# Performance work log

Hardware: AMD Instinct MI355X
Metric: run time of the kernel (lower is better)

Reference implementation:

```python
import jax, jax.numpy as jnp
import numpy as np

NB, NA, NC, NH, NW = 32, 5, 80, 64, 64
MAXT = 50
STRIDE = 32.0
ANCHORS_PX = [42.3, 55.4, 102.2, 128.3, 161.8, 259.2, 303.1, 154.9, 359.6, 320.2]
NOOBJECT_SCALE, OBJECT_SCALE = 1.0, 5.0
COORD_SCALE, CLASS_SCALE = 1.0, 1.0
SIL_THRESH = 0.6


def _iou_center(ax, ay, aw, ah, bx, by, bw, bh):
    # IoU for boxes in (cx, cy, w, h) form; zero when no overlap (matches bbox_ious x1y1x2y2=False)
    iw = jnp.minimum(ax + aw * 0.5, bx + bw * 0.5) - jnp.maximum(ax - aw * 0.5, bx - bw * 0.5)
    ih = jnp.minimum(ay + ah * 0.5, by + bh * 0.5) - jnp.maximum(ay - ah * 0.5, by - bh * 0.5)
    inter = jnp.maximum(iw, 0.0) * jnp.maximum(ih, 0.0)
    union = aw * ah + bw * bh - inter
    return inter / union


def _region_loss(output, target):
    sg = jax.lax.stop_gradient
    anchors = jnp.array(ANCHORS_PX, jnp.float32).reshape(NA, 2) / STRIDE  # anchors scaled by stride
    out = output.reshape(NB, NA, 5 + NC, NH, NW)
    x = jax.nn.sigmoid(out[:, :, 0])
    y = jax.nn.sigmoid(out[:, :, 1])
    w = out[:, :, 2]
    h = out[:, :, 3]
    conf = jax.nn.sigmoid(out[:, :, 4])
    cls_logits = jnp.transpose(out[:, :, 5:], (0, 1, 3, 4, 2))  # [B,A,H,W,C]

    grid_x = jnp.arange(NW, dtype=jnp.float32)[None, None, None, :]
    grid_y = jnp.arange(NH, dtype=jnp.float32)[None, None, :, None]
    aw = anchors[:, 0][None, :, None, None]
    ah = anchors[:, 1][None, :, None, None]
    # decoded pred boxes are detached in the torch code (built from .data)
    px = sg(x) + grid_x
    py = sg(y) + grid_y
    pw = jnp.exp(sg(w)) * aw
    ph = jnp.exp(sg(h)) * ah

    tgt = sg(target).reshape(NB, MAXT, 5)  # [cls, x, y, w, h] per target, normalized
    gcls = tgt[:, :, 0]
    gx = tgt[:, :, 1] * NW
    gy = tgt[:, :, 2] * NH
    gw = tgt[:, :, 3] * NW
    gh = tgt[:, :, 4] * NH
    # loop breaks at first target with x == 0 -> cumulative validity
    valid = jnp.cumprod((tgt[:, :, 1] != 0).astype(jnp.float32), axis=1) > 0  # [B,T]

    # --- conf mask silencing: max IoU of each pred box against all GT boxes ---
    ious = _iou_center(px[..., None], py[..., None], pw[..., None], ph[..., None],
                       gx[:, None, None, None, :], gy[:, None, None, None, :],
                       gw[:, None, None, None, :], gh[:, None, None, None, :])  # [B,A,H,W,T]
    ious = jnp.where(valid[:, None, None, None, :], ious, 0.0)
    cur_ious = jnp.max(ious, axis=-1)
    conf_mask0 = jnp.where(cur_ious > SIL_THRESH, 0.0, NOOBJECT_SCALE)

    # --- best anchor per GT: wh-only IoU at origin (anchor_step == 2) ---
    inter = jnp.minimum(gw[..., None], anchors[None, None, :, 0]) * \
            jnp.minimum(gh[..., None], anchors[None, None, :, 1])  # [B,T,A]
    union = gw[..., None] * gh[..., None] + anchors[None, None, :, 0] * anchors[None, None, :, 1] - inter
    best_n = jnp.argmax(inter / union, axis=-1)

    gi = jnp.clip(gx.astype(jnp.int32), 0, NW - 1)
    gj = jnp.clip(gy.astype(jnp.int32), 0, NH - 1)
    bidx = jnp.arange(NB, dtype=jnp.int32)[:, None]
    aw_b = anchors[best_n, 0]
    ah_b = anchors[best_n, 1]

    pb_x = px[bidx, best_n, gj, gi]
    pb_y = py[bidx, best_n, gj, gi]
    pb_w = pw[bidx, best_n, gj, gi]
    pb_h = ph[bidx, best_n, gj, gi]
    t_iou = _iou_center(gx, gy, gw, gh, pb_x, pb_y, pb_w, pb_h)  # [B,T]

    N = NB * NA * NH * NW
    flat = ((bidx * NA + best_n) * NH + gj) * NW + gi
    flat = jnp.where(valid, flat, N).reshape(-1)  # invalid targets scattered to dummy slot

    def scat(base, vals):
        padded = jnp.concatenate([base.reshape(-1), jnp.zeros((1,), base.dtype)])
        return padded.at[flat].set(vals.reshape(-1))[:N].reshape(NB, NA, NH, NW)

    ones_t = jnp.ones_like(gx)
    # seen=0 < 12800 -> coord_mask = 1 everywhere, tx=ty=0.5, tw=th=0 as base
    coord_mask = scat(jnp.ones((NB, NA, NH, NW), jnp.float32), ones_t)
    cls_mask = scat(jnp.zeros((NB, NA, NH, NW), jnp.float32), ones_t)
    conf_mask = scat(conf_mask0, jnp.full_like(gx, OBJECT_SCALE))
    txg = scat(jnp.full((NB, NA, NH, NW), 0.5, jnp.float32), gx - gi.astype(jnp.float32))
    tyg = scat(jnp.full((NB, NA, NH, NW), 0.5, jnp.float32), gy - gj.astype(jnp.float32))
    twg = scat(jnp.zeros((NB, NA, NH, NW), jnp.float32), jnp.log(gw / aw_b))
    thg = scat(jnp.zeros((NB, NA, NH, NW), jnp.float32), jnp.log(gh / ah_b))
    tconf = scat(jnp.zeros((NB, NA, NH, NW), jnp.float32), t_iou)
    tcls = scat(jnp.zeros((NB, NA, NH, NW), jnp.float32), gcls)

    conf_m = jnp.sqrt(conf_mask)
    loss_x = COORD_SCALE * jnp.sum((x * coord_mask - txg * coord_mask) ** 2) / 2.0
    loss_y = COORD_SCALE * jnp.sum((y * coord_mask - tyg * coord_mask) ** 2) / 2.0
    loss_w = COORD_SCALE * jnp.sum((w * coord_mask - twg * coord_mask) ** 2) / 2.0
    loss_h = COORD_SCALE * jnp.sum((h * coord_mask - thg * coord_mask) ** 2) / 2.0
    loss_conf = jnp.sum((conf * conf_m - tconf * conf_m) ** 2) / 2.0
    # CrossEntropy over cells where cls_mask == 1 (sum reduction)
    logZ = jax.nn.logsumexp(cls_logits, axis=-1)
    picked = jnp.take_along_axis(cls_logits, tcls.astype(jnp.int32)[..., None], axis=-1)[..., 0]
    loss_cls = CLASS_SCALE * jnp.sum((logZ - picked) * cls_mask)
    return loss_x + loss_y + loss_w + loss_h + loss_conf + loss_cls


def setup_inputs() -> dict:
    key = jax.random.key(0)
    k1, k2, k3, k4 = jax.random.split(key, 4)
    output = jax.random.normal(k1, (NB, NA * (5 + NC), NH, NW), jnp.float32) * 0.5
    cls_ids = jax.random.randint(k2, (NB, MAXT), 0, NC).astype(jnp.float32)
    xy = jax.random.uniform(k3, (NB, MAXT, 2), jnp.float32, minval=0.05, maxval=0.95)
    wh = jax.random.uniform(k4, (NB, MAXT, 2), jnp.float32, minval=0.05, maxval=0.4)
    target = jnp.concatenate([cls_ids[..., None], xy, wh], axis=-1).reshape(NB, MAXT * 5)
    return {"output": output, "target": target}


def reference(output, target):
    return _region_loss(output, target)
```

## Files before the change

kernel.cpp:

```cpp
#include <hip/hip_runtime.h>

#define NB 32
#define NA 5
#define NC 80
#define NH 64
#define NW 64
#define MAXT 50
#define CH 85
#define HW (NH*NW)
#define NCELL (NB*NA*HW)

#define TGT_BASE 16
#define TGT_STRIDE 336
#define ENT_BASE (TGT_BASE + NB*TGT_STRIDE)
#define ENT_STRIDE (8 + 8*MAXT)
#define T_XLO 16
#define T_XHI 80
#define T_YLO 144
#define T_YHI 208
#define T_GA  272

__constant__ float c_aw[NA] = {42.3f/32.0f, 102.2f/32.0f, 161.8f/32.0f, 303.1f/32.0f, 359.6f/32.0f};
__constant__ float c_ah[NA] = {55.4f/32.0f, 128.3f/32.0f, 259.2f/32.0f, 154.9f/32.0f, 320.2f/32.0f};

__device__ __forceinline__ float sigm(float x) {
    return __builtin_amdgcn_rcpf(1.0f + __expf(-x));
}

__global__ void prep_kernel(const float* __restrict__ out, const float* __restrict__ tgt,
                            float* __restrict__ W) {
    const int b = blockIdx.x;
    const int t = threadIdx.x;
    if (b == 0 && t == 0) W[0] = 0.0f;

    __shared__ int s_id[MAXT];

    bool iszero = true;
    float gcls = 0.f, gx = 0.f, gy = 0.f, gw = 0.f, gh = 0.f;
    if (t < MAXT) {
        const float* p = tgt + (b*MAXT + t)*5;
        gcls = p[0];
        float rx = p[1];
        iszero = (rx == 0.0f);
        gx = rx * (float)NW;
        gy = p[2] * (float)NH;
        gw = p[3] * (float)NW;
        gh = p[4] * (float)NH;
    }
    unsigned long long mz = __ballot(iszero);
    const int nvalid = __ffsll(mz) - 1;

    float* TB = W + TGT_BASE + (size_t)b*TGT_STRIDE;

    int   myid = -1;
    float tx = 0.f, ty = 0.f, tw = 0.f, th = 0.f, tiou = 0.f;
    int   mycl = 0;

    if (t < MAXT) {
        TB[T_XLO + t] = gx - 0.5f*gw;
        TB[T_XHI + t] = gx + 0.5f*gw;
        TB[T_YLO + t] = gy - 0.5f*gh;
        TB[T_YHI + t] = gy + 0.5f*gh;
        TB[T_GA  + t] = 0.375f * gw * gh;

        float garea = gw * gh;
        float best = -1.0f; int bn = 0;
        #pragma unroll
        for (int n = 0; n < NA; n++) {
            float inter = fminf(gw, c_aw[n]) * fminf(gh, c_ah[n]);
            float uni = garea + c_aw[n]*c_ah[n] - inter;
            float r = inter / uni;
            if (r > best) { best = r; bn = n; }
        }
        int gi = (int)gx; gi = gi < 0 ? 0 : (gi > NW-1 ? NW-1 : gi);
        int gj = (int)gy; gj = gj < 0 ? 0 : (gj > NH-1 ? NH-1 : gj);
        float awb = c_aw[bn], ahb = c_ah[bn];

        int base = ((b*NA + bn)*CH)*HW + gj*NW + gi;
        float ox = out[base];
        float oy = out[base + HW];
        float ow = out[base + 2*HW];
        float oh = out[base + 3*HW];
        float px = sigm(ox) + (float)gi;
        float py = sigm(oy) + (float)gj;
        float pw = __expf(ow) * awb;
        float ph = __expf(oh) * ahb;
        float iw = fminf(gx + 0.5f*gw, px + 0.5f*pw) - fmaxf(gx - 0.5f*gw, px - 0.5f*pw);
        float ih = fminf(gy + 0.5f*gh, py + 0.5f*ph) - fmaxf(gy - 0.5f*gh, py - 0.5f*ph);
        float inter = fmaxf(iw, 0.f) * fmaxf(ih, 0.f);
        tiou = inter / (garea + pw*ph - inter);

        myid = (bn*NH + gj)*NW + gi;
        tx = gx - (float)gi;
        ty = gy - (float)gj;
        tw = __logf(gw / awb);
        th = __logf(gh / ahb);
        mycl = (int)gcls;
        s_id[t] = myid;
    }
    __syncthreads();

    bool keepf = (t < nvalid);
    if (keepf) {
        for (int u = t + 1; u < nvalid; u++) {
            if (s_id[u] == myid) { keepf = false; break; }
        }
    }

    float* EB = W + ENT_BASE + (size_t)b*ENT_STRIDE;
    if (t == 0) {
        ((int*)TB)[0] = nvalid;
        ((int*)EB)[0] = nvalid;
    }
    if (t < nvalid) {
        float* e = EB + 8 + t*8;
        ((int*)e)[0] = keepf ? myid : -1;
        e[1] = tx; e[2] = ty; e[3] = tw; e[4] = th; e[5] = tiou;
        ((int*)e)[6] = mycl;
    }
}

__global__ __launch_bounds__(256) void main_kernel(const float* __restrict__ out,
                                                   float* __restrict__ W) {
    const int cell = blockIdx.x * 256 + threadIdx.x;
    const int b = cell / (NA*HW);
    const int rem = cell - b*(NA*HW);
    const int a = rem / HW;
    const int ji = rem & (HW-1);
    const int i = ji & (NW-1);
    const int j = ji >> 6;

    __shared__ float sxl[MAXT], sxh[MAXT], syl[MAXT], syh[MAXT], sga[MAXT];
    __shared__ int s_nv;
    const float* TB = W + TGT_BASE + (size_t)b*TGT_STRIDE;
    if (threadIdx.x == 0) s_nv = ((const int*)TB)[0];
    if (threadIdx.x < MAXT) {
        int t = threadIdx.x;
        sxl[t] = TB[T_XLO+t]; sxh[t] = TB[T_XHI+t];
        syl[t] = TB[T_YLO+t]; syh[t] = TB[T_YHI+t];
        sga[t] = TB[T_GA+t];
    }
    __syncthreads();

    const size_t base = (size_t)((b*NA + a)*CH)*HW + ji;
    const float ox = out[base];
    const float oy = out[base + HW];
    const float ow = out[base + 2*HW];
    const float oh = out[base + 3*HW];
    const float oc = out[base + 4*HW];

    const float sx = sigm(ox);
    const float sy = sigm(oy);
    const float sc = sigm(oc);
    const float pw = __expf(ow) * c_aw[a];
    const float ph = __expf(oh) * c_ah[a];
    const float px = sx + (float)i;
    const float py = sy + (float)j;
    const float pxl = px - 0.5f*pw, pxh = px + 0.5f*pw;
    const float pyl = py - 0.5f*ph, pyh = py + 0.5f*ph;
    const float pa375 = 0.375f * pw * ph;

    const int nv = s_nv;
    float m = -1.0f;
    for (int tt = 0; tt < nv; tt++) {
        float iw = fminf(pxh, sxh[tt]) - fmaxf(pxl, sxl[tt]);
        float ih = fminf(pyh, syh[tt]) - fmaxf(pyl, syl[tt]);
        float inter = fmaxf(iw, 0.f) * fmaxf(ih, 0.f);
        m = fmaxf(m, inter - sga[tt]);
    }
    const bool over = m > pa375;

    const float dx = sx - 0.5f, dy = sy - 0.5f;
    float v = dx*dx + dy*dy + ow*ow + oh*oh;
    if (!over) v += sc*sc;
    v *= 0.5f;

    for (int off = 32; off > 0; off >>= 1) v += __shfl_down(v, off);
    __shared__ float red[4];
    if ((threadIdx.x & 63) == 0) red[threadIdx.x >> 6] = v;
    __syncthreads();
    if (threadIdx.x == 0) atomicAdd(W, red[0]+red[1]+red[2]+red[3]);
}

__global__ void corr_kernel(const float* __restrict__ out, float* __restrict__ W) {
    const int b = blockIdx.x;
    const int t = threadIdx.x;
    __shared__ float sxl[MAXT], sxh[MAXT], syl[MAXT], syh[MAXT], sga[MAXT];
    const float* TB = W + TGT_BASE + (size_t)b*TGT_STRIDE;
    const int nv = ((const int*)TB)[0];
    if (t < MAXT) {
        sxl[t] = TB[T_XLO+t]; sxh[t] = TB[T_XHI+t];
        syl[t] = TB[T_YLO+t]; syh[t] = TB[T_YHI+t];
        sga[t] = TB[T_GA+t];
    }
    __syncthreads();
    const float* EB = W + ENT_BASE + (size_t)b*ENT_STRIDE;
    const int cnt = ((const int*)EB)[0];
    float acc = 0.f;
    for (int e = t; e < cnt; e += 64) {
        const float* en = EB + 8 + e*8;
        const int id = ((const int*)en)[0];
        if (id < 0) continue;
        const float tx = en[1], ty = en[2], tw = en[3], th = en[4], ti = en[5];
        const int cls = ((const int*)en)[6];
        const int a = id >> 12;
        const int ji = id & (HW-1);
        const int i = ji & (NW-1);
        const int j = ji >> 6;
        const size_t base = (size_t)((b*NA + a)*CH)*HW + ji;
        const float ox = out[base];
        const float oy = out[base + HW];
        const float ow = out[base + 2*HW];
        const float oh = out[base + 3*HW];
        const float oc = out[base + 4*HW];
        const float sx = sigm(ox), sy = sigm(oy), sc = sigm(oc);

        const float dxn = sx - tx, dxo = sx - 0.5f;
        const float dyn = sy - ty, dyo = sy - 0.5f;
        const float dwn = ow - tw, dhn = oh - th;
        float d = dxn*dxn - dxo*dxo + dyn*dyn - dyo*dyo + dwn*dwn - ow*ow + dhn*dhn - oh*oh;

        const float pw = __expf(ow) * c_aw[a];
        const float ph = __expf(oh) * c_ah[a];
        const float px = sx + (float)i, py = sy + (float)j;
        const float pxl = px - 0.5f*pw, pxh = px + 0.5f*pw;
        const float pyl = py - 0.5f*ph, pyh = py + 0.5f*ph;
        const float pa375 = 0.375f * pw * ph;
        float mm = -1.0f;
        for (int u = 0; u < nv; u++) {
            float iw = fminf(pxh, sxh[u]) - fmaxf(pxl, sxl[u]);
            float ih = fminf(pyh, syh[u]) - fmaxf(pyl, syl[u]);
            float inter = fmaxf(iw, 0.f) * fmaxf(ih, 0.f);
            mm = fmaxf(mm, inter - sga[u]);
        }
        float dc = 5.f*(sc - ti)*(sc - ti);
        if (!(mm > pa375)) dc -= sc*sc;
        d += dc;
        acc += 0.5f * d;

        const float* lg = out + base + 5*HW;
        float mx = lg[0];
        for (int c = 1; c < NC; c++) mx = fmaxf(mx, lg[(size_t)c*HW]);
        float s = 0.f;
        for (int c = 0; c < NC; c++) s += __expf(lg[(size_t)c*HW] - mx);
        acc += mx + __logf(s) - lg[(size_t)cls*HW];
    }
    for (int off = 32; off > 0; off >>= 1) acc += __shfl_down(acc, off);
    if (t == 0) atomicAdd(W, acc);
}

__global__ void fin_kernel(const float* __restrict__ W, float* __restrict__ res) {
    res[0] = W[0];
}

extern "C" void kernel_launch(void* const* d_in, const int* in_sizes, int n_in,
                              void* d_out, int out_size, void* d_ws, size_t ws_size,
                              hipStream_t stream) {
    const float* out = (const float*)d_in[0];
    const float* tgt = (const float*)d_in[1];
    float* W = (float*)d_ws;
    float* res = (float*)d_out;
    hipLaunchKernelGGL(prep_kernel, dim3(NB), dim3(64), 0, stream, out, tgt, W);
    hipLaunchKernelGGL(main_kernel, dim3(NCELL/256), dim3(256), 0, stream, out, W);
    hipLaunchKernelGGL(corr_kernel, dim3(NB), dim3(64), 0, stream, out, W);
    hipLaunchKernelGGL(fin_kernel, dim3(1), dim3(1), 0, stream, W, res);
}
```

Baseline: 331.7 us.

## Fuse prep, main and correction kernels into one pass with per-block partials

Merges the target-prep, per-cell conf loss, and per-target correction kernels into a single kernel. Each block recomputes target boxes in shared memory, and the first block of each image also does the correction work, splitting the class logsumexp across 4 lanes per target. The global atomic is replaced by per-block partial sums that a final kernel reduces. This removes two launches and the serial correction kernel, but every block now redundantly reads the targets and the r==0 blocks carry extra work.

```diff
diff --git a/kernel.cpp b/kernel.cpp
--- a/kernel.cpp
+++ b/kernel.cpp
@@ -8,17 +8,8 @@
 #define MAXT 50
 #define CH 85
 #define HW (NH*NW)
-#define NCELL (NB*NA*HW)
-
-#define TGT_BASE 16
-#define TGT_STRIDE 336
-#define ENT_BASE (TGT_BASE + NB*TGT_STRIDE)
-#define ENT_STRIDE (8 + 8*MAXT)
-#define T_XLO 16
-#define T_XHI 80
-#define T_YLO 144
-#define T_YHI 208
-#define T_GA  272
+#define NBLK (NB*NA*HW/256)
+#define BPB (NA*HW/256)
 
 __constant__ float c_aw[NA] = {42.3f/32.0f, 102.2f/32.0f, 161.8f/32.0f, 303.1f/32.0f, 359.6f/32.0f};
 __constant__ float c_ah[NA] = {55.4f/32.0f, 128.3f/32.0f, 259.2f/32.0f, 154.9f/32.0f, 320.2f/32.0f};
@@ -27,120 +18,48 @@
     return __builtin_amdgcn_rcpf(1.0f + __expf(-x));
 }
 
-__global__ void prep_kernel(const float* __restrict__ out, const float* __restrict__ tgt,
-                            float* __restrict__ W) {
-    const int b = blockIdx.x;
-    const int t = threadIdx.x;
-    if (b == 0 && t == 0) W[0] = 0.0f;
-
-    __shared__ int s_id[MAXT];
-
-    bool iszero = true;
-    float gcls = 0.f, gx = 0.f, gy = 0.f, gw = 0.f, gh = 0.f;
-    if (t < MAXT) {
-        const float* p = tgt + (b*MAXT + t)*5;
-        gcls = p[0];
-        float rx = p[1];
-        iszero = (rx == 0.0f);
-        gx = rx * (float)NW;
-        gy = p[2] * (float)NH;
-        gw = p[3] * (float)NW;
-        gh = p[4] * (float)NH;
-    }
-    unsigned long long mz = __ballot(iszero);
-    const int nvalid = __ffsll(mz) - 1;
-
-    float* TB = W + TGT_BASE + (size_t)b*TGT_STRIDE;
-
-    int   myid = -1;
-    float tx = 0.f, ty = 0.f, tw = 0.f, th = 0.f, tiou = 0.f;
-    int   mycl = 0;
-
-    if (t < MAXT) {
-        TB[T_XLO + t] = gx - 0.5f*gw;
-        TB[T_XHI + t] = gx + 0.5f*gw;
-        TB[T_YLO + t] = gy - 0.5f*gh;
-        TB[T_YHI + t] = gy + 0.5f*gh;
-        TB[T_GA  + t] = 0.375f * gw * gh;
-
-        float garea = gw * gh;
-        float best = -1.0f; int bn = 0;
-        #pragma unroll
-        for (int n = 0; n < NA; n++) {
-            float inter = fminf(gw, c_aw[n]) * fminf(gh, c_ah[n]);
-            float uni = garea + c_aw[n]*c_ah[n] - inter;
-            float r = inter / uni;
-            if (r > best) { best = r; bn = n; }
-        }
-        int gi = (int)gx; gi = gi < 0 ? 0 : (gi > NW-1 ? NW-1 : gi);
-        int gj = (int)gy; gj = gj < 0 ? 0 : (gj > NH-1 ? NH-1 : gj);
-        float awb = c_aw[bn], ahb = c_ah[bn];
-
-        int base = ((b*NA + bn)*CH)*HW + gj*NW + gi;
-        float ox = out[base];
-        float oy = out[base + HW];
-        float ow = out[base + 2*HW];
-        float oh = out[base + 3*HW];
-        float px = sigm(ox) + (float)gi;
-        float py = sigm(oy) + (float)gj;
-        float pw = __expf(ow) * awb;
-        float ph = __expf(oh) * ahb;
-        float iw = fminf(gx + 0.5f*gw, px + 0.5f*pw) - fmaxf(gx - 0.5f*gw, px - 0.5f*pw);
-        float ih = fminf(gy + 0.5f*gh, py + 0.5f*ph) - fmaxf(gy - 0.5f*gh, py - 0.5f*ph);
-        float inter = fmaxf(iw, 0.f) * fmaxf(ih, 0.f);
-        tiou = inter / (garea + pw*ph - inter);
-
-        myid = (bn*NH + gj)*NW + gi;
-        tx = gx - (float)gi;
-        ty = gy - (float)gj;
-        tw = __logf(gw / awb);
-        th = __logf(gh / ahb);
-        mycl = (int)gcls;
-        s_id[t] = myid;
+__global__ __launch_bounds__(256) void fused_kernel(const float* __restrict__ out,
+                                                    const float* __restrict__ tgt,
+                                                    float* __restrict__ W) {
+    const int blk = blockIdx.x;
+    const int tid = threadIdx.x;
+    const int b   = blk / BPB;
+    const int r   = blk - b*BPB;
+    const int a   = r >> 4;
+    const int ji  = ((r & 15) << 8) + tid;
+    const int i   = ji & (NW-1);
+    const int j   = ji >> 6;
+
+    __shared__ float sxl[MAXT], sxh[MAXT], syl[MAXT], syh[MAXT], sga[MAXT];
+    __shared__ float sgx[MAXT], sgy[MAXT], sgw[MAXT], sgh[MAXT], sgc[MAXT];
+    __shared__ int   s_id[MAXT];
+    __shared__ int   s_eid[MAXT];
+    __shared__ float s_tx[MAXT], s_ty[MAXT], s_tw[MAXT], s_th[MAXT], s_ti[MAXT];
+    __shared__ int   s_ec[MAXT];
+    __shared__ int   s_nv;
+    __shared__ float red[4];
+
+    if (tid < 64) {
+        bool iszero = true;
+        if (tid < MAXT) {
+            const float* p = tgt + (b*MAXT + tid)*5;
+            const float gcls = p[0];
+            const float rx = p[1];
+            iszero = (rx == 0.0f);
+            const float gx = rx   * (float)NW;
+            const float gy = p[2] * (float)NH;
+            const float gw = p[3] * (float)NW;
+            const float gh = p[4] * (float)NH;
+            sxl[tid] = gx - 0.5f*gw; sxh[tid] = gx + 0.5f*gw;
+            syl[tid] = gy - 0.5f*gh; syh[tid] = gy + 0.5f*gh;
+            sga[tid] = 0.375f*gw*gh;
+            sgx[tid] = gx; sgy[tid] = gy; sgw[tid] = gw; sgh[tid] = gh; sgc[tid] = gcls;
+        }
+        unsigned long long mz = __ballot(iszero);
+        if (tid == 0) s_nv = __ffsll(mz) - 1;
     }
     __syncthreads();
-
-    bool keepf = (t < nvalid);
-    if (keepf) {
-        for (int u = t + 1; u < nvalid; u++) {
-            if (s_id[u] == myid) { keepf = false; break; }
-        }
-    }
-
-    float* EB = W + ENT_BASE + (size_t)b*ENT_STRIDE;
-    if (t == 0) {
-        ((int*)TB)[0] = nvalid;
-        ((int*)EB)[0] = nvalid;
-    }
-    if (t < nvalid) {
-        float* e = EB + 8 + t*8;
-        ((int*)e)[0] = keepf ? myid : -1;
-        e[1] = tx; e[2] = ty; e[3] = tw; e[4] = th; e[5] = tiou;
-        ((int*)e)[6] = mycl;
-    }
-}
-
-__global__ __launch_bounds__(256) void main_kernel(const float* __restrict__ out,
-                                                   float* __restrict__ W) {
-    const int cell = blockIdx.x * 256 + threadIdx.x;
-    const int b = cell / (NA*HW);
-    const int rem = cell - b*(NA*HW);
-    const int a = rem / HW;
-    const int ji = rem & (HW-1);
-    const int i = ji & (NW-1);
-    const int j = ji >> 6;
-
-    __shared__ float sxl[MAXT], sxh[MAXT], syl[MAXT], syh[MAXT], sga[MAXT];
-    __shared__ int s_nv;
-    const float* TB = W + TGT_BASE + (size_t)b*TGT_STRIDE;
-    if (threadIdx.x == 0) s_nv = ((const int*)TB)[0];
-    if (threadIdx.x < MAXT) {
-        int t = threadIdx.x;
-        sxl[t] = TB[T_XLO+t]; sxh[t] = TB[T_XHI+t];
-        syl[t] = TB[T_YLO+t]; syh[t] = TB[T_YHI+t];
-        sga[t] = TB[T_GA+t];
-    }
-    __syncthreads();
+    const int nv = s_nv;
 
     const size_t base = (size_t)((b*NA + a)*CH)*HW + ji;
     const float ox = out[base];
@@ -160,7 +79,6 @@
     const float pyl = py - 0.5f*ph, pyh = py + 0.5f*ph;
     const float pa375 = 0.375f * pw * ph;
 
-    const int nv = s_nv;
     float m = -1.0f;
     for (int tt = 0; tt < nv; tt++) {
         float iw = fminf(pxh, sxh[tt]) - fmaxf(pxl, sxl[tt]);
@@ -176,81 +94,141 @@
     v *= 0.5f;
 
     for (int off = 32; off > 0; off >>= 1) v += __shfl_down(v, off);
+    if ((tid & 63) == 0) red[tid >> 6] = v;
+    __syncthreads();
+    float bsum = (tid == 0) ? (red[0] + red[1] + red[2] + red[3]) : 0.0f;
+
+    if (r == 0) {
+        if (tid < 64 && tid < nv) {
+            const float gx = sgx[tid], gy = sgy[tid], gw = sgw[tid], gh = sgh[tid];
+            const float garea = gw * gh;
+            float best = -1.0f; int bn = 0;
+            #pragma unroll
+            for (int n = 0; n < NA; n++) {
+                float inter = fminf(gw, c_aw[n]) * fminf(gh, c_ah[n]);
+                float uni = garea + c_aw[n]*c_ah[n] - inter;
+                float rr = inter / uni;
+                if (rr > best) { best = rr; bn = n; }
+            }
+            int gi = (int)gx; gi = gi < 0 ? 0 : (gi > NW-1 ? NW-1 : gi);
+            int gj = (int)gy; gj = gj < 0 ? 0 : (gj > NH-1 ? NH-1 : gj);
+            const float awb = c_aw[bn], ahb = c_ah[bn];
+
+            const size_t gbase = (size_t)((b*NA + bn)*CH)*HW + gj*NW + gi;
+            const float o0 = out[gbase];
+            const float o1 = out[gbase + HW];
+            const float o2 = out[gbase + 2*HW];
+            const float o3 = out[gbase + 3*HW];
+            const float ppx = sigm(o0) + (float)gi;
+            const float ppy = sigm(o1) + (float)gj;
+            const float ppw = __expf(o2) * awb;
+            const float pph = __expf(o3) * ahb;
+            const float iw = fminf(gx + 0.5f*gw, ppx + 0.5f*ppw) - fmaxf(gx - 0.5f*gw, ppx - 0.5f*ppw);
+            const float ih = fminf(gy + 0.5f*gh, ppy + 0.5f*pph) - fmaxf(gy - 0.5f*gh, ppy - 0.5f*pph);
+            const float inter = fmaxf(iw, 0.f) * fmaxf(ih, 0.f);
+            const float tiou = inter / (garea + ppw*pph - inter);
+
+            s_id[tid] = (bn*NH + gj)*NW + gi;
+            s_tx[tid] = gx - (float)gi;
+            s_ty[tid] = gy - (float)gj;
+            s_tw[tid] = __logf(gw / awb);
+            s_th[tid] = __logf(gh / ahb);
+            s_ti[tid] = tiou;
+            s_ec[tid] = (int)sgc[tid];
+        }
+        __syncthreads();
+        if (tid < nv) {
+            const int myid = s_id[tid];
+            bool keep = true;
+            for (int u = tid + 1; u < nv; u++)
+                if (s_id[u] == myid) { keep = false; break; }
+            s_eid[tid] = keep ? myid : -1;
+        }
+        __syncthreads();
+
+        float acc = 0.0f;
+        const int e = tid >> 2;
+        const int q = tid & 3;
+        if (e < nv) {
+            const int id = s_eid[e];
+            if (id >= 0) {
+                const int ea  = id >> 12;
+                const int eji = id & (HW-1);
+                const int eii = eji & (NW-1);
+                const int ejj = eji >> 6;
+                const size_t eb = (size_t)((b*NA + ea)*CH)*HW + eji;
+                const float cox = out[eb];
+                const float coy = out[eb + HW];
+                const float cow = out[eb + 2*HW];
+                const float coh = out[eb + 3*HW];
+                const float coc = out[eb + 4*HW];
+                const float csx = sigm(cox), csy = sigm(coy), csc = sigm(coc);
+                const float cpw = __expf(cow) * c_aw[ea];
+                const float cph = __expf(coh) * c_ah[ea];
+                const float cpx = csx + (float)eii, cpy = csy + (float)ejj;
+                const float cxl = cpx - 0.5f*cpw, cxh = cpx + 0.5f*cpw;
+                const float cyl = cpy - 0.5f*cph, cyh = cpy + 0.5f*cph;
+                const float cpa = 0.375f * cpw * cph;
+
+                float mm = -1.0f;
+                for (int u = q; u < nv; u += 4) {
+                    float iw = fminf(cxh, sxh[u]) - fmaxf(cxl, sxl[u]);
+                    float ih = fminf(cyh, syh[u]) - fmaxf(cyl, syl[u]);
+                    float inter = fmaxf(iw, 0.f) * fmaxf(ih, 0.f);
+                    mm = fmaxf(mm, inter - sga[u]);
+                }
+                mm = fmaxf(mm, __shfl_xor(mm, 1));
+                mm = fmaxf(mm, __shfl_xor(mm, 2));
+
+                const float* lg = out + eb + 5*HW;
+                float rch[20];
+                #pragma unroll
+                for (int k = 0; k < 20; k++) rch[k] = lg[(size_t)(q + 4*k)*HW];
+                float mx = rch[0];
+                #pragma unroll
+                for (int k = 1; k < 20; k++) mx = fmaxf(mx, rch[k]);
+                mx = fmaxf(mx, __shfl_xor(mx, 1));
+                mx = fmaxf(mx, __shfl_xor(mx, 2));
+                float s = 0.0f;
+                #pragma unroll
+                for (int k = 0; k < 20; k++) s += __expf(rch[k] - mx);
+                s += __shfl_xor(s, 1);
+                s += __shfl_xor(s, 2);
+
+                if (q == 0) {
+                    const float tx = s_tx[e], ty = s_ty[e], tw = s_tw[e], th = s_th[e], ti = s_ti[e];
+                    const int cls = s_ec[e];
+                    const float dxn = csx - tx, dxo = csx - 0.5f;
+                    const float dyn = csy - ty, dyo = csy - 0.5f;
+                    const float dwn = cow - tw, dhn = coh - th;
+                    float d = dxn*dxn - dxo*dxo + dyn*dyn - dyo*dyo
+                            + dwn*dwn - cow*cow + dhn*dhn - coh*coh;
+                    float dc = 5.f*(csc - ti)*(csc - ti);
+                    if (!(mm > cpa)) dc -= csc*csc;
+                    d += dc;
+                    acc += 0.5f * d;
+                    acc += mx + __logf(s) - lg[(size_t)cls*HW];
+                }
+            }
+        }
+        for (int off = 32; off > 0; off >>= 1) acc += __shfl_down(acc, off);
+        if ((tid & 63) == 0) red[tid >> 6] = acc;
+        __syncthreads();
+        if (tid == 0) bsum += red[0] + red[1] + red[2] + red[3];
+    }
+
+    if (tid == 0) W[blk] = bsum;
+}
+
+__global__ __launch_bounds__(256) void fin_kernel(const float* __restrict__ W,
+                                                  float* __restrict__ res) {
+    float s = 0.0f;
+    for (int k = threadIdx.x; k < NBLK; k += 256) s += W[k];
+    for (int off = 32; off > 0; off >>= 1) s += __shfl_down(s, off);
     __shared__ float red[4];
-    if ((threadIdx.x & 63) == 0) red[threadIdx.x >> 6] = v;
+    if ((threadIdx.x & 63) == 0) red[threadIdx.x >> 6] = s;
     __syncthreads();
-    if (threadIdx.x == 0) atomicAdd(W, red[0]+red[1]+red[2]+red[3]);
-}
-
-__global__ void corr_kernel(const float* __restrict__ out, float* __restrict__ W) {
-    const int b = blockIdx.x;
-    const int t = threadIdx.x;
-    __shared__ float sxl[MAXT], sxh[MAXT], syl[MAXT], syh[MAXT], sga[MAXT];
-    const float* TB = W + TGT_BASE + (size_t)b*TGT_STRIDE;
-    const int nv = ((const int*)TB)[0];
-    if (t < MAXT) {
-        sxl[t] = TB[T_XLO+t]; sxh[t] = TB[T_XHI+t];
-        syl[t] = TB[T_YLO+t]; syh[t] = TB[T_YHI+t];
-        sga[t] = TB[T_GA+t];
-    }
-    __syncthreads();
-    const float* EB = W + ENT_BASE + (size_t)b*ENT_STRIDE;
-    const int cnt = ((const int*)EB)[0];
-    float acc = 0.f;
-    for (int e = t; e < cnt; e += 64) {
-        const float* en = EB + 8 + e*8;
-        const int id = ((const int*)en)[0];
-        if (id < 0) continue;
-        const float tx = en[1], ty = en[2], tw = en[3], th = en[4], ti = en[5];
-        const int cls = ((const int*)en)[6];
-        const int a = id >> 12;
-        const int ji = id & (HW-1);
-        const int i = ji & (NW-1);
-        const int j = ji >> 6;
-        const size_t base = (size_t)((b*NA + a)*CH)*HW + ji;
-        const float ox = out[base];
-        const float oy = out[base + HW];
-        const float ow = out[base + 2*HW];
-        const float oh = out[base + 3*HW];
-        const float oc = out[base + 4*HW];
-        const float sx = sigm(ox), sy = sigm(oy), sc = sigm(oc);
-
-        const float dxn = sx - tx, dxo = sx - 0.5f;
-        const float dyn = sy - ty, dyo = sy - 0.5f;
-        const float dwn = ow - tw, dhn = oh - th;
-        float d = dxn*dxn - dxo*dxo + dyn*dyn - dyo*dyo + dwn*dwn - ow*ow + dhn*dhn - oh*oh;
-
-        const float pw = __expf(ow) * c_aw[a];
-        const float ph = __expf(oh) * c_ah[a];
-        const float px = sx + (float)i, py = sy + (float)j;
-        const float pxl = px - 0.5f*pw, pxh = px + 0.5f*pw;
-        const float pyl = py - 0.5f*ph, pyh = py + 0.5f*ph;
-        const float pa375 = 0.375f * pw * ph;
-        float mm = -1.0f;
-        for (int u = 0; u < nv; u++) {
-            float iw = fminf(pxh, sxh[u]) - fmaxf(pxl, sxl[u]);
-            float ih = fminf(pyh, syh[u]) - fmaxf(pyl, syl[u]);
-            float inter = fmaxf(iw, 0.f) * fmaxf(ih, 0.f);
-            mm = fmaxf(mm, inter - sga[u]);
-        }
-        float dc = 5.f*(sc - ti)*(sc - ti);
-        if (!(mm > pa375)) dc -= sc*sc;
-        d += dc;
-        acc += 0.5f * d;
-
-        const float* lg = out + base + 5*HW;
-        float mx = lg[0];
-        for (int c = 1; c < NC; c++) mx = fmaxf(mx, lg[(size_t)c*HW]);
-        float s = 0.f;
-        for (int c = 0; c < NC; c++) s += __expf(lg[(size_t)c*HW] - mx);
-        acc += mx + __logf(s) - lg[(size_t)cls*HW];
-    }
-    for (int off = 32; off > 0; off >>= 1) acc += __shfl_down(acc, off);
-    if (t == 0) atomicAdd(W, acc);
-}
-
-__global__ void fin_kernel(const float* __restrict__ W, float* __restrict__ res) {
-    res[0] = W[0];
+    if (threadIdx.x == 0) res[0] = red[0] + red[1] + red[2] + red[3];
 }
 
 extern "C" void kernel_launch(void* const* d_in, const int* in_sizes, int n_in,
@@ -260,8 +238,6 @@
     const float* tgt = (const float*)d_in[1];
     float* W = (float*)d_ws;
     float* res = (float*)d_out;
-    hipLaunchKernelGGL(prep_kernel, dim3(NB), dim3(64), 0, stream, out, tgt, W);
-    hipLaunchKernelGGL(main_kernel, dim3(NCELL/256), dim3(256), 0, stream, out, W);
-    hipLaunchKernelGGL(corr_kernel, dim3(NB), dim3(64), 0, stream, out, W);
-    hipLaunchKernelGGL(fin_kernel, dim3(1), dim3(1), 0, stream, W, res);
-}
+    hipLaunchKernelGGL(fused_kernel, dim3(NBLK), dim3(256), 0, stream, out, tgt, W);
+    hipLaunchKernelGGL(fin_kernel, dim3(1), dim3(256), 0, stream, W, res);
+}
```

New measurement: 300.8 us. 9.3% less time.
